# Optimization experiments

Hardware: AMD Instinct MI355X
Metric: run time of the kernel (lower is better)

The kernel has to match this reference:

```python
import jax, jax.numpy as jnp
import numpy as np

D = 2048
H = 16
DK = D // H
B = 2
S = 2048


def setup_inputs() -> dict:
    key = jax.random.key(0)
    ks = jax.random.split(key, 11)
    s = 1.0 / np.sqrt(D)
    inp = {
        "q": jax.random.normal(ks[0], (B, S, D), jnp.float32),
        "k": jax.random.normal(ks[1], (B, S, D), jnp.float32),
        "v": jax.random.normal(ks[2], (B, S, D), jnp.float32),
        "mask": 0,
        "Wq": jax.random.normal(ks[3], (D, D), jnp.float32) * s,
        "bq": jax.random.normal(ks[4], (D,), jnp.float32) * s,
        "Wk": jax.random.normal(ks[5], (D, D), jnp.float32) * s,
        "bk": jax.random.normal(ks[6], (D,), jnp.float32) * s,
        "Wv": jax.random.normal(ks[7], (D, D), jnp.float32) * s,
        "bv": jax.random.normal(ks[8], (D,), jnp.float32) * s,
        "Wo": jax.random.normal(ks[9], (D, D), jnp.float32) * s,
        "bo": jax.random.normal(ks[10], (D,), jnp.float32) * s,
    }
    return inp


def reference(q, k, v, mask, Wq, bq, Wk, bk, Wv, bv, Wo, bo):
    # Linear projections (torch Linear: x @ W.T + b)
    query = q @ Wq.T + bq  # [B,S,D]
    key_ = k @ Wk.T + bk
    value = v @ Wv.T + bv
    # split heads -> [B,S,H,DK]
    query = query.reshape(B, S, H, DK)
    key_ = key_.reshape(B, S, H, DK)
    value = value.reshape(B, S, H, DK)
    # scores [B,H,Sq,Sk]
    scores = jnp.einsum('nqhd,nkhd->nhqk', query, key_)
    if mask:
        # faithful to source: fill where triu(ones, diag=1) == 0 (lower tri incl diag)
        tri = jnp.triu(jnp.ones((S, S), jnp.float32), k=1)
        scores = jnp.where(tri == 0, jnp.float32(-1e20), scores)
    attn = jax.nn.softmax(scores / np.sqrt(DK), axis=3)
    # dropout=0.0 -> identity
    out = jnp.einsum('nhql,nlhd->nqhd', attn, value).reshape(B, S, D)
    return out @ Wo.T + bo
```

## Files before the change

kernel.cpp:

```cpp
#include <hip/hip_runtime.h>
#include <math.h>

typedef unsigned short u16;
typedef u16 u16x8 __attribute__((ext_vector_type(8)));
typedef u16 u16x4 __attribute__((ext_vector_type(4)));
typedef short s16x8 __attribute__((ext_vector_type(8)));
typedef short s16x4 __attribute__((ext_vector_type(4)));
typedef float f32x4 __attribute__((ext_vector_type(4)));

static constexpr int B_ = 2;
static constexpr int S_ = 2048;
static constexpr int D_ = 2048;
static constexpr int H_ = 16;
static constexpr int DK = 128;
static constexpr long long BSD = (long long)B_ * S_ * D_;
static constexpr long long DD  = (long long)D_ * D_;

#if __has_builtin(__builtin_amdgcn_mfma_f32_16x16x32_bf16)
#define HAVE_MFMA32 1
#else
#define HAVE_MFMA32 0
#endif
#if __has_builtin(__builtin_amdgcn_mfma_f32_16x16x16bf16_1k)
#define HAVE_MFMA16 1
#else
#define HAVE_MFMA16 0
#endif

__device__ __forceinline__ u16 f2bf(float f) {
    union { float f; unsigned u; } cv; cv.f = f;
    unsigned u = cv.u;
    return (u16)((u + 0x7fffu + ((u >> 16) & 1u)) >> 16);
}

__device__ __forceinline__ unsigned pack2bf(float a, float b) {
    union { float f; unsigned u; } x, y; x.f = a; y.f = b;
    return ((y.u + 0x8000u) & 0xffff0000u) | ((x.u + 0x8000u) >> 16);
}

__device__ __forceinline__ f32x4 mfma32(f32x4 c, u16x8 a, u16x8 b) {
#if HAVE_MFMA32
    return __builtin_amdgcn_mfma_f32_16x16x32_bf16((s16x8)a, (s16x8)b, c, 0, 0, 0);
#else
    asm volatile("v_mfma_f32_16x16x32_bf16 %0, %1, %2, %0" : "+v"(c) : "v"(a), "v"(b));
    return c;
#endif
}
__device__ __forceinline__ f32x4 mfma16(f32x4 c, u16x4 a, u16x4 b) {
#if HAVE_MFMA16
    return __builtin_amdgcn_mfma_f32_16x16x16bf16_1k((s16x4)a, (s16x4)b, c, 0, 0, 0);
#else
    asm volatile("v_mfma_f32_16x16x16_bf16 %0, %1, %2, %0" : "+v"(c) : "v"(a), "v"(b));
    return c;
#endif
}
__device__ __forceinline__ void fenceB() {
#if !HAVE_MFMA32 || !HAVE_MFMA16
    asm volatile("s_nop 7\ns_nop 7" :::);
#endif
}

__device__ __forceinline__ void glds16(const u16* g, u16* l) {
    __builtin_amdgcn_global_load_lds(
        (const __attribute__((address_space(1))) unsigned int*)g,
        (__attribute__((address_space(3))) unsigned int*)l, 16, 0, 0);
}

__device__ __forceinline__ float fexp2(float x) {
#if __has_builtin(__builtin_amdgcn_exp2f)
    return __builtin_amdgcn_exp2f(x);
#else
    return exp2f(x);
#endif
}

struct CastArgs {
    const float* src[7];
    u16* dst[7];
    int start[8];
};
__global__ __launch_bounds__(256) void cast_all(CastArgs a) {
    int g = blockIdx.x * 256 + threadIdx.x;
    if (g >= a.start[7]) return;
    int seg = 0;
#pragma unroll
    for (int i = 1; i < 7; ++i) seg += (g >= a.start[i]) ? 1 : 0;
    int idx = g - a.start[seg];
    float4 f = ((const float4*)a.src[seg])[idx];
    ushort4 o;
    o.x = f2bf(f.x); o.y = f2bf(f.y); o.z = f2bf(f.z); o.w = f2bf(f.w);
    ((ushort4*)a.dst[seg])[idx] = o;
}

#define GEMM_K64_LOOP(Aptr, Bptr)                                                   \
    for (int k0 = 0; k0 < D_; k0 += 64) {                                           \
        __syncthreads();                                                            \
        _Pragma("unroll")                                                           \
        for (int s = 0; s < 4; ++s) {                                               \
            int slot = s * 256 + t;                                                 \
            int row = slot >> 3;                                                    \
            int c = (t & 7) ^ (row & 7);                                            \
            glds16(Aptr + (m0 + row) * D_ + k0 + c * 8, &As[slot * 8]);             \
        }                                                                           \
        _Pragma("unroll")                                                           \
        for (int s = 0; s < 4; ++s) {                                               \
            int slot = s * 256 + t;                                                 \
            int row = slot >> 3;                                                    \
            int c = (t & 7) ^ (row & 7);                                            \
            glds16(Bptr + (n0 + row) * D_ + k0 + c * 8, &Bs[slot * 8]);             \
        }                                                                           \
        __syncthreads();                                                            \
        u16x8 af[4][2], bf[4][2];                                                   \
        _Pragma("unroll")                                                           \
        for (int i = 0; i < 4; ++i) {                                               \
            int row = wm + i * 16 + l16;                                            \
            _Pragma("unroll")                                                       \
            for (int kk = 0; kk < 2; ++kk)                                          \
                af[i][kk] = *(const u16x8*)(&As[row * 64 +                          \
                                (((kk * 4 + quad) ^ (row & 7)) * 8)]);              \
        }                                                                           \
        _Pragma("unroll")                                                           \
        for (int j = 0; j < 4; ++j) {                                               \
            int row = wn + j * 16 + l16;                                            \
            _Pragma("unroll")                                                       \
            for (int kk = 0; kk < 2; ++kk)                                          \
                bf[j][kk] = *(const u16x8*)(&Bs[row * 64 +                          \
                                (((kk * 4 + quad) ^ (row & 7)) * 8)]);              \
        }                                                                           \
        _Pragma("unroll")                                                           \
        for (int kk = 0; kk < 2; ++kk)                                              \
            _Pragma("unroll")                                                       \
            for (int i = 0; i < 4; ++i)                                             \
                _Pragma("unroll")                                                   \
                for (int j = 0; j < 4; ++j)                                         \
                    acc[i][j] = mfma32(acc[i][j], af[i][kk], bf[j][kk]);            \
    }

struct QkvArgs {
    const u16* X[3];
    const u16* W[3];
    const float* bias[3];
    u16* outQ;
    u16* outK;
    u16* outVt;
    float scaleQ;
};
__global__ __launch_bounds__(256) void qkv_proj(QkvArgs a) {
    __shared__ u16 SM[16384];
    u16* As = SM;
    u16* Bs = SM + 8192;

    const int zsel = blockIdx.z;
    const u16* A = a.X[zsel];
    const u16* Bw = a.W[zsel];
    const float scale = (zsel == 0) ? a.scaleQ : 1.0f;

    const int t = threadIdx.x;
    const int wave = t >> 6, lane = t & 63;
    const int quad = lane >> 4, l16 = lane & 15;
    const int wm = (wave >> 1) * 64;
    const int wn = (wave & 1) * 64;
    const long long m0 = (long long)blockIdx.y * 128;
    const long long n0 = (long long)blockIdx.x * 128;

    f32x4 acc[4][4];
#pragma unroll
    for (int i = 0; i < 4; ++i)
#pragma unroll
        for (int j = 0; j < 4; ++j)
            acc[i][j] = f32x4{0.f, 0.f, 0.f, 0.f};

    GEMM_K64_LOOP(A, Bw)

    fenceB();

    float bs[4];
#pragma unroll
    for (int j = 0; j < 4; ++j)
        bs[j] = a.bias[zsel][(int)n0 + wn + j * 16 + l16];

    if (zsel < 2) {
        u16* C = (zsel == 0) ? a.outQ : a.outK;
#pragma unroll
        for (int p = 0; p < 2; ++p) {
            __syncthreads();
#pragma unroll
            for (int jj = 0; jj < 2; ++jj) {
                int j = p * 2 + jj;
#pragma unroll
                for (int i = 0; i < 4; ++i)
#pragma unroll
                    for (int r = 0; r < 4; ++r) {
                        int row = wm + i * 16 + quad * 4 + r;
                        int lc = (wave & 1) * 32 + jj * 16 + l16;
                        SM[row * 64 + lc] = f2bf((acc[i][j][r] + bs[j]) * scale);
                    }
            }
            __syncthreads();
#pragma unroll
            for (int i = 0; i < 4; ++i) {
                int idx = i * 256 + t;
                int row = idx >> 3, cc = idx & 7;
                u16x8 val = *(const u16x8*)(&SM[row * 64 + cc * 8]);
                long long n = n0 + 32 * p + (cc & 3) * 8 + (cc >> 2) * 64;
                *(u16x8*)(C + (m0 + row) * (long long)D_ + n) = val;
            }
        }
    } else {
        const int h = blockIdx.x;
        const int b = (int)(m0 >> 11);
        const int tok0 = (int)(m0 & 2047);
        const int z = b * 16 + h;
        u16* vt = a.outVt + (long long)z * DK * S_;
#pragma unroll
        for (int p = 0; p < 2; ++p) {
            __syncthreads();
#pragma unroll
            for (int jj = 0; jj < 2; ++jj) {
                int j = p * 2 + jj;
#pragma unroll
                for (int i = 0; i < 4; ++i)
#pragma unroll
                    for (int r = 0; r < 4; ++r) {
                        int row = wm + i * 16 + quad * 4 + r;
                        int lc = (wave & 1) * 32 + jj * 16 + l16;
                        SM[lc * 136 + row] = f2bf(acc[i][j][r] + bs[j]);
                    }
            }
            __syncthreads();
#pragma unroll
            for (int i = 0; i < 4; ++i) {
                int idx = i * 256 + t;
                int lc2 = idx >> 4, cc = idx & 15;
                int d = p * 32 + (lc2 & 31) + (lc2 >> 5) * 64;
                u16x8 val = *(const u16x8*)(&SM[lc2 * 136 + cc * 8]);
                *(u16x8*)(vt + (long long)d * S_ + tok0 + cc * 8) = val;
            }
        }
    }
}

__global__ __launch_bounds__(256) void gemm_out(const u16* __restrict__ Ain,
                                                const u16* __restrict__ Bin,
                                                float* __restrict__ C,
                                                const float* __restrict__ bias) {
    __shared__ u16 SM[16384];
    u16* As = SM;
    u16* Bs = SM + 8192;

    const int t = threadIdx.x;
    const int wave = t >> 6, lane = t & 63;
    const int quad = lane >> 4, l16 = lane & 15;
    const int wm = (wave >> 1) * 64;
    const int wn = (wave & 1) * 64;
    const long long m0 = (long long)blockIdx.y * 128;
    const long long n0 = (long long)blockIdx.x * 128;

    f32x4 acc[4][4];
#pragma unroll
    for (int i = 0; i < 4; ++i)
#pragma unroll
        for (int j = 0; j < 4; ++j)
            acc[i][j] = f32x4{0.f, 0.f, 0.f, 0.f};

    GEMM_K64_LOOP(Ain, Bin)

    fenceB();

    float bs[4];
#pragma unroll
    for (int j = 0; j < 4; ++j)
        bs[j] = bias[(int)n0 + wn + j * 16 + l16];

    float* Cf = (float*)SM;
#pragma unroll
    for (int p = 0; p < 2; ++p) {
        __syncthreads();
#pragma unroll
        for (int jj = 0; jj < 2; ++jj) {
            int j = p * 2 + jj;
#pragma unroll
            for (int i = 0; i < 4; ++i)
#pragma unroll
                for (int r = 0; r < 4; ++r) {
                    int row = wm + i * 16 + quad * 4 + r;
                    int lc = (wave & 1) * 32 + jj * 16 + l16;
                    Cf[row * 64 + lc] = acc[i][j][r] + bs[j];
                }
        }
        __syncthreads();
#pragma unroll
        for (int i = 0; i < 8; ++i) {
            int idx = i * 256 + t;
            int row = idx >> 4, c4 = idx & 15;
            f32x4 val = *(const f32x4*)(&Cf[row * 64 + c4 * 4]);
            long long n = n0 + (c4 >> 3) * 64 + p * 32 + (c4 & 7) * 4;
            *(f32x4*)(C + (m0 + row) * (long long)D_ + n) = val;
        }
    }
}

__global__ __launch_bounds__(256, 2) void flash_attn(const u16* __restrict__ Qb,
                                                     const u16* __restrict__ Kb,
                                                     const u16* __restrict__ Vt,
                                                     u16* __restrict__ Ob) {
    __shared__ u16 Ks[2][64 * 128];
    __shared__ u16 Vs[2][128 * 64];

    const int z  = blockIdx.x;
    const int qt = blockIdx.y;
    const int b  = z >> 4, h = z & 15;
    const int t = threadIdx.x, wave = t >> 6, lane = t & 63;
    const int quad = lane >> 4, l16 = lane & 15;

    const u16* kbase = Kb + (long long)(b * S_) * D_ + h * DK;
    const u16* vbase = Vt + (long long)z * DK * S_;

    u16x8 qf[2][4];
    {
        const u16* qbase = Qb + ((long long)(b * S_ + qt * 128 + wave * 32 + l16)) * D_
                              + h * DK + quad * 8;
#pragma unroll
        for (int jq = 0; jq < 2; ++jq)
#pragma unroll
            for (int kk = 0; kk < 4; ++kk)
                qf[jq][kk] = *(const u16x8*)(qbase + (long long)jq * 16 * D_ + kk * 32);
    }

    f32x4 acc_o[2][8];
#pragma unroll
    for (int jq = 0; jq < 2; ++jq)
#pragma unroll
        for (int jd = 0; jd < 8; ++jd)
            acc_o[jq][jd] = f32x4{0.f, 0.f, 0.f, 0.f};
    float l_[2] = {0.f, 0.f};

    u16x8 vreg[4];

    {
#pragma unroll
        for (int i = 0; i < 4; ++i) {
            int slot = i * 256 + t;
            int row = slot >> 3, c16 = slot & 7;
            vreg[i] = *(const u16x8*)(vbase + (long long)row * S_ + c16 * 8);
        }
#pragma unroll
        for (int i = 0; i < 4; ++i) {
            int slot = i * 256 + t;
            int row = slot >> 4;
            int cs = (slot & 15) ^ (row & 7);
            glds16(kbase + (long long)row * D_ + cs * 8, &Ks[0][slot * 8]);
        }
#pragma unroll
        for (int i = 0; i < 4; ++i) {
            int slot = i * 256 + t;
            int row = slot >> 3, c16 = slot & 7;
            int rm = row & 15;
            u16x4 lo = __builtin_shufflevector(vreg[i], vreg[i], 0, 1, 2, 3);
            u16x4 hi = __builtin_shufflevector(vreg[i], vreg[i], 4, 5, 6, 7);
            *(u16x4*)(&Vs[0][row * 64 + (((2 * c16) ^ rm) * 4)]) = lo;
            *(u16x4*)(&Vs[0][row * 64 + (((2 * c16 + 1) ^ rm) * 4)]) = hi;
        }
    }

    for (int kt = 0; kt < S_ / 64; ++kt) {
        __syncthreads();
        const int p = kt & 1;
        const u16* ks = Ks[p];
        const u16* vs = Vs[p];
        const bool pre = (kt + 1) < (S_ / 64);
        if (pre) {
            const u16* vsrc = vbase + (kt + 1) * 64;
#pragma unroll
            for (int i = 0; i < 4; ++i) {
                int slot = i * 256 + t;
                int row = slot >> 3, c16 = slot & 7;
                vreg[i] = *(const u16x8*)(vsrc + (long long)row * S_ + c16 * 8);
            }
            const u16* ksrc = kbase + (long long)(kt + 1) * 64 * D_;
#pragma unroll
            for (int i = 0; i < 4; ++i) {
                int slot = i * 256 + t;
                int row = slot >> 4;
                int cs = (slot & 15) ^ (row & 7);
                glds16(ksrc + (long long)row * D_ + cs * 8, &Ks[p ^ 1][slot * 8]);
            }
        }

        f32x4 st[4][2];
#pragma unroll
        for (int ik = 0; ik < 4; ++ik)
#pragma unroll
            for (int jq = 0; jq < 2; ++jq)
                st[ik][jq] = f32x4{0.f, 0.f, 0.f, 0.f};
#pragma unroll
        for (int kk = 0; kk < 4; ++kk) {
            u16x8 kf[4];
#pragma unroll
            for (int ik = 0; ik < 4; ++ik) {
                int krow = ik * 16 + l16;
                kf[ik] = *(const u16x8*)(&ks[krow * 128 + (((kk * 4 + quad) ^ (l16 & 7)) * 8)]);
            }
#pragma unroll
            for (int ik = 0; ik < 4; ++ik) {
                st[ik][0] = mfma32(st[ik][0], kf[ik], qf[0][kk]);
                st[ik][1] = mfma32(st[ik][1], kf[ik], qf[1][kk]);
            }
        }
        fenceB();

        if (pre) {
#pragma unroll
            for (int i = 0; i < 4; ++i) {
                int slot = i * 256 + t;
                int row = slot >> 3, c16 = slot & 7;
                int rm = row & 15;
                u16x4 lo = __builtin_shufflevector(vreg[i], vreg[i], 0, 1, 2, 3);
                u16x4 hi = __builtin_shufflevector(vreg[i], vreg[i], 4, 5, 6, 7);
                *(u16x4*)(&Vs[p ^ 1][row * 64 + (((2 * c16) ^ rm) * 4)]) = lo;
                *(u16x4*)(&Vs[p ^ 1][row * 64 + (((2 * c16 + 1) ^ rm) * 4)]) = hi;
            }
        }

        u16x4 pf[4][2];
#pragma unroll
        for (int ik = 0; ik < 4; ++ik)
#pragma unroll
            for (int jq = 0; jq < 2; ++jq) {
                float p0 = fexp2(st[ik][jq][0]);
                float p1 = fexp2(st[ik][jq][1]);
                float p2 = fexp2(st[ik][jq][2]);
                float p3 = fexp2(st[ik][jq][3]);
                l_[jq] += (p0 + p1) + (p2 + p3);
                union { u16x4 v; unsigned u[2]; } pk;
                pk.u[0] = pack2bf(p0, p1);
                pk.u[1] = pack2bf(p2, p3);
                pf[ik][jq] = pk.v;
            }

#pragma unroll
        for (int ik = 0; ik < 4; ++ik) {
            const int kc = ik * 4 + quad;
            u16x4 vf[8];
#pragma unroll
            for (int jd = 0; jd < 8; ++jd) {
                int vrow = jd * 16 + l16;
                vf[jd] = *(const u16x4*)(&vs[vrow * 64 + ((kc ^ l16) * 4)]);
            }
#pragma unroll
            for (int jd = 0; jd < 8; ++jd) {
                acc_o[0][jd] = mfma16(acc_o[0][jd], pf[ik][0], vf[jd]);
                acc_o[1][jd] = mfma16(acc_o[1][jd], pf[ik][1], vf[jd]);
            }
        }
        fenceB();
    }

    float lr[2][4];
#pragma unroll
    for (int jq = 0; jq < 2; ++jq) {
        float s = l_[jq];
        s += __shfl_xor(s, 16, 64);
        s += __shfl_xor(s, 32, 64);
        float inv = 1.f / s;
#pragma unroll
        for (int r = 0; r < 4; ++r)
            lr[jq][r] = __shfl(inv, quad * 20 + r, 64);
    }
    u16* OS = (u16*)Ks;
    __syncthreads();
#pragma unroll
    for (int jq = 0; jq < 2; ++jq)
#pragma unroll
        for (int r = 0; r < 4; ++r) {
            int qloc = wave * 32 + jq * 16 + quad * 4 + r;
#pragma unroll
            for (int jd = 0; jd < 8; ++jd)
                OS[qloc * 128 + jd * 16 + l16] = f2bf(acc_o[jq][jd][r] * lr[jq][r]);
        }
    __syncthreads();
    u16* obase = Ob + ((long long)(b * S_ + qt * 128)) * D_ + h * DK;
#pragma unroll
    for (int i = 0; i < 8; ++i) {
        int idx = i * 256 + t;
        int row = idx >> 4, cc = idx & 15;
        *(u16x8*)(obase + (long long)row * D_ + cc * 8) = *(const u16x8*)(&OS[row * 128 + cc * 8]);
    }
}

extern "C" void kernel_launch(void* const* d_in, const int* in_sizes, int n_in,
                              void* d_out, int out_size, void* d_ws, size_t ws_size,
                              hipStream_t stream) {
    const float* q  = (const float*)d_in[0];
    const float* k  = (const float*)d_in[1];
    const float* v  = (const float*)d_in[2];
    const float* Wq = (const float*)d_in[4];
    const float* bq = (const float*)d_in[5];
    const float* Wk = (const float*)d_in[6];
    const float* bk = (const float*)d_in[7];
    const float* Wv = (const float*)d_in[8];
    const float* bv = (const float*)d_in[9];
    const float* Wo = (const float*)d_in[10];
    const float* bo = (const float*)d_in[11];
    float* out = (float*)d_out;

    u16* ws = (u16*)d_ws;
    u16* xq  = ws; ws += BSD;
    u16* xk  = ws; ws += BSD;
    u16* xv  = ws; ws += BSD;
    u16* wqb = ws; ws += DD;
    u16* wkb = ws; ws += DD;
    u16* wvb = ws; ws += DD;
    u16* wob = ws; ws += DD;
    u16* Qb  = ws; ws += BSD;
    u16* Kb  = ws; ws += BSD;
    u16* Vt  = ws; ws += BSD;
    u16* Ob  = ws; ws += BSD;

    const float q_scale = (float)(0.08838834764831845 * 1.4426950408889634);

    {
        CastArgs a;
        const float* srcs[7] = {q, k, v, Wq, Wk, Wv, Wo};
        u16* dsts[7] = {xq, xk, xv, wqb, wkb, wvb, wob};
        int n4s[7] = {(int)(BSD / 4), (int)(BSD / 4), (int)(BSD / 4),
                      (int)(DD / 4), (int)(DD / 4), (int)(DD / 4), (int)(DD / 4)};
        int acc = 0;
        for (int i = 0; i < 7; ++i) { a.src[i] = srcs[i]; a.dst[i] = dsts[i]; a.start[i] = acc; acc += n4s[i]; }
        a.start[7] = acc;
        cast_all<<<(acc + 255) / 256, 256, 0, stream>>>(a);
    }

    {
        QkvArgs a;
        a.X[0] = xq;  a.X[1] = xk;  a.X[2] = xv;
        a.W[0] = wqb; a.W[1] = wkb; a.W[2] = wvb;
        a.bias[0] = bq; a.bias[1] = bk; a.bias[2] = bv;
        a.outQ = Qb; a.outK = Kb; a.outVt = Vt;
        a.scaleQ = q_scale;
        qkv_proj<<<dim3(D_ / 128, (B_ * S_) / 128, 3), 256, 0, stream>>>(a);
    }

    flash_attn<<<dim3(B_ * H_, S_ / 128), 256, 0, stream>>>(Qb, Kb, Vt, Ob);

    gemm_out<<<dim3(D_ / 128, (B_ * S_) / 128), 256, 0, stream>>>(Ob, wob, out, bo);
}
```

Baseline: 446.7 us.

## Rewrite QKV projection as 256x256-tile, 8-wave double-buffered GEMM with swizzled LDS

Replaces the 128x128 QKV projection kernel with a 512-thread kernel computing 256x256 output tiles. It double-buffers A and B tiles in 128 KB of LDS via direct global-to-LDS loads with an XOR swizzle, and interleaves the loads with MFMA phases using explicit waitcnt, barriers and setprio. The aim is more operand reuse per loaded byte, fewer bank conflicts and overlap of memory with math. The trade-off is high register and LDS pressure: there are 32 accumulators per wave, and 128 KB of LDS per block probably means one block per CU. The epilogues are also rewritten for the larger tile.

```diff
diff --git a/kernel.cpp b/kernel.cpp
--- a/kernel.cpp
+++ b/kernel.cpp
@@ -74,6 +74,16 @@
 #endif
 }
 
+__device__ __forceinline__ void cfence() { asm volatile("" ::: "memory"); }
+__device__ __forceinline__ void barrier8() {
+    cfence();
+    __builtin_amdgcn_s_barrier();
+    cfence();
+}
+#define LGKM0() do { asm volatile("s_waitcnt lgkmcnt(0)" ::: "memory"); \
+                     __builtin_amdgcn_sched_barrier(0); } while (0)
+#define VMC(N)  asm volatile("s_waitcnt vmcnt(" #N ")" ::: "memory")
+
 struct CastArgs {
     const float* src[7];
     u16* dst[7];
@@ -145,96 +155,188 @@
     u16* outVt;
     float scaleQ;
 };
-__global__ __launch_bounds__(256) void qkv_proj(QkvArgs a) {
-    __shared__ u16 SM[16384];
-    u16* As = SM;
-    u16* Bs = SM + 8192;
+
+#define STAGE_HALF(LDS, GBASE)                                                      \
+    _Pragma("unroll")                                                               \
+    for (int jj = 0; jj < 2; ++jj) {                                                \
+        int slot = jj * 512 + t;                                                    \
+        int row = slot >> 3, c = slot & 7;                                          \
+        glds16((GBASE) + (long long)row * D_ + ((c ^ (row & 7)) * 8),               \
+               (LDS) + slot * 8);                                                   \
+    }
+
+#define RD_A(QM, LDSA)                                                              \
+    _Pragma("unroll")                                                               \
+    for (int i2 = 0; i2 < 4; ++i2) {                                                \
+        int row = wm128 + (QM) * 64 + i2 * 16 + l16;                                \
+        _Pragma("unroll")                                                           \
+        for (int kk = 0; kk < 2; ++kk)                                              \
+            af[(QM) * 4 + i2][kk] = *(const u16x8*)(&(LDSA)[row * 64 +              \
+                                (((kk * 4 + quad) ^ (row & 7)) * 8)]);              \
+    }
+
+#define RD_B(QN, LDSB)                                                              \
+    _Pragma("unroll")                                                               \
+    for (int j2 = 0; j2 < 2; ++j2) {                                                \
+        int row = wn64 + (QN) * 32 + j2 * 16 + l16;                                 \
+        _Pragma("unroll")                                                           \
+        for (int kk = 0; kk < 2; ++kk)                                              \
+            bf[j2][kk] = *(const u16x8*)(&(LDSB)[row * 64 +                         \
+                                (((kk * 4 + quad) ^ (row & 7)) * 8)]);              \
+    }
+
+#define MM(QM, QN)                                                                  \
+    __builtin_amdgcn_s_setprio(1);                                                  \
+    _Pragma("unroll")                                                               \
+    for (int kk = 0; kk < 2; ++kk)                                                  \
+        _Pragma("unroll")                                                           \
+        for (int i2 = 0; i2 < 4; ++i2)                                              \
+            _Pragma("unroll")                                                       \
+            for (int j2 = 0; j2 < 2; ++j2)                                          \
+                acc[(QM) * 4 + i2][(QN) * 2 + j2] =                                 \
+                    mfma32(acc[(QM) * 4 + i2][(QN) * 2 + j2],                       \
+                           af[(QM) * 4 + i2][kk], bf[j2][kk]);                      \
+    __builtin_amdgcn_s_setprio(0);
+
+__global__ __launch_bounds__(512, 2) void qkv_proj8(QkvArgs a) {
+    __shared__ u16 SM8[65536];
+    u16* const As0 = SM8;
+    u16* const As1 = SM8 + 16384;
+    u16* const Bs0 = SM8 + 32768;
+    u16* const Bs1 = SM8 + 49152;
 
     const int zsel = blockIdx.z;
-    const u16* A = a.X[zsel];
-    const u16* Bw = a.W[zsel];
-    const float scale = (zsel == 0) ? a.scaleQ : 1.0f;
+    const u16* __restrict__ Ag = a.X[zsel];
+    const u16* __restrict__ Bg = a.W[zsel];
 
     const int t = threadIdx.x;
-    const int wave = t >> 6, lane = t & 63;
+    const int lane = t & 63;
     const int quad = lane >> 4, l16 = lane & 15;
-    const int wm = (wave >> 1) * 64;
-    const int wn = (wave & 1) * 64;
-    const long long m0 = (long long)blockIdx.y * 128;
-    const long long n0 = (long long)blockIdx.x * 128;
-
-    f32x4 acc[4][4];
-#pragma unroll
-    for (int i = 0; i < 4; ++i)
+    const int wave = t >> 6;
+    const int wm128 = (wave >> 2) * 128;
+    const int wn64  = (wave & 3) * 64;
+    const long long m0 = (long long)blockIdx.y * 256;
+    const long long n0 = (long long)blockIdx.x * 256;
+
+    f32x4 acc[8][4];
+#pragma unroll
+    for (int i = 0; i < 8; ++i)
 #pragma unroll
         for (int j = 0; j < 4; ++j)
             acc[i][j] = f32x4{0.f, 0.f, 0.f, 0.f};
 
-    GEMM_K64_LOOP(A, Bw)
-
+    u16x8 af[8][2];
+    u16x8 bf[2][2];
+
+    STAGE_HALF(As0,         Ag + m0 * D_)
+    STAGE_HALF(As0 + 8192,  Ag + (m0 + 128) * D_)
+    STAGE_HALF(Bs0,         Bg + n0 * D_)
+    STAGE_HALF(Bs0 + 8192,  Bg + (n0 + 128) * D_)
+    STAGE_HALF(As1,         Ag + m0 * D_ + 64)
+    STAGE_HALF(As1 + 8192,  Ag + (m0 + 128) * D_ + 64)
+    VMC(4);
+    barrier8();
+
+#pragma unroll 1
+    for (int it = 0; it < 16; ++it) {
+        const int E = 2 * it;
+        const bool more = (it < 15);
+        const long long kO  = (long long)(E + 1) * 64;
+        const long long kE2 = (long long)(E + 2) * 64;
+        const long long kO2 = (long long)(E + 3) * 64;
+
+        RD_A(0, As0) RD_B(0, Bs0)
+        STAGE_HALF(Bs1,        Bg + n0 * D_ + kO)
+        barrier8(); LGKM0(); MM(0, 0) barrier8();
+
+        RD_A(1, As0) RD_B(1, Bs0)
+        STAGE_HALF(Bs1 + 8192, Bg + (n0 + 128) * D_ + kO)
+        barrier8(); LGKM0(); MM(0, 1) barrier8();
+
+        RD_B(0, Bs0)
+        if (more) { STAGE_HALF(As0,        Ag + m0 * D_ + kE2) }
+        barrier8(); LGKM0(); MM(1, 0) barrier8();
+
+        RD_B(1, Bs0)
+        if (more) { STAGE_HALF(As0 + 8192, Ag + (m0 + 128) * D_ + kE2) }
+        barrier8(); LGKM0(); MM(1, 1)
+        if (more) { VMC(4); } else { VMC(0); }
+        barrier8();
+
+        RD_A(0, As1) RD_B(0, Bs1)
+        if (more) { STAGE_HALF(Bs0,        Bg + n0 * D_ + kE2) }
+        barrier8(); LGKM0(); MM(0, 0) barrier8();
+
+        RD_A(1, As1) RD_B(1, Bs1)
+        if (more) { STAGE_HALF(Bs0 + 8192, Bg + (n0 + 128) * D_ + kE2) }
+        barrier8(); LGKM0(); MM(0, 1) barrier8();
+
+        RD_B(0, Bs1)
+        if (more) { STAGE_HALF(As1,        Ag + m0 * D_ + kO2) }
+        barrier8(); LGKM0(); MM(1, 0) barrier8();
+
+        RD_B(1, Bs1)
+        if (more) { STAGE_HALF(As1 + 8192, Ag + (m0 + 128) * D_ + kO2) }
+        barrier8(); LGKM0(); MM(1, 1)
+        if (more) { VMC(4); }
+        barrier8();
+    }
     fenceB();
 
     float bs[4];
 #pragma unroll
     for (int j = 0; j < 4; ++j)
-        bs[j] = a.bias[zsel][(int)n0 + wn + j * 16 + l16];
+        bs[j] = a.bias[zsel][(int)n0 + wn64 + j * 16 + l16];
 
     if (zsel < 2) {
+        const float scale = (zsel == 0) ? a.scaleQ : 1.0f;
         u16* C = (zsel == 0) ? a.outQ : a.outK;
 #pragma unroll
-        for (int p = 0; p < 2; ++p) {
-            __syncthreads();
-#pragma unroll
-            for (int jj = 0; jj < 2; ++jj) {
-                int j = p * 2 + jj;
-#pragma unroll
-                for (int i = 0; i < 4; ++i)
-#pragma unroll
-                    for (int r = 0; r < 4; ++r) {
-                        int row = wm + i * 16 + quad * 4 + r;
-                        int lc = (wave & 1) * 32 + jj * 16 + l16;
-                        SM[row * 64 + lc] = f2bf((acc[i][j][r] + bs[j]) * scale);
-                    }
-            }
-            __syncthreads();
-#pragma unroll
-            for (int i = 0; i < 4; ++i) {
-                int idx = i * 256 + t;
-                int row = idx >> 3, cc = idx & 7;
-                u16x8 val = *(const u16x8*)(&SM[row * 64 + cc * 8]);
-                long long n = n0 + 32 * p + (cc & 3) * 8 + (cc >> 2) * 64;
-                *(u16x8*)(C + (m0 + row) * (long long)D_ + n) = val;
-            }
+        for (int i = 0; i < 8; ++i)
+#pragma unroll
+            for (int j = 0; j < 4; ++j)
+#pragma unroll
+                for (int r = 0; r < 4; ++r) {
+                    int row = wm128 + i * 16 + quad * 4 + r;
+                    int col = wn64 + j * 16 + l16;
+                    SM8[row * 256 + col] = f2bf((acc[i][j][r] + bs[j]) * scale);
+                }
+        barrier8();
+#pragma unroll
+        for (int s = 0; s < 16; ++s) {
+            int idx = s * 512 + t;
+            int row = idx >> 5, c = idx & 31;
+            *(u16x8*)(C + (m0 + row) * (long long)D_ + n0 + c * 8) =
+                *(const u16x8*)(&SM8[row * 256 + c * 8]);
         }
     } else {
-        const int h = blockIdx.x;
-        const int b = (int)(m0 >> 11);
+        const int h0 = (int)(n0 >> 7);
+        const int bb = (int)(m0 >> 11);
         const int tok0 = (int)(m0 & 2047);
-        const int z = b * 16 + h;
-        u16* vt = a.outVt + (long long)z * DK * S_;
-#pragma unroll
-        for (int p = 0; p < 2; ++p) {
-            __syncthreads();
-#pragma unroll
-            for (int jj = 0; jj < 2; ++jj) {
-                int j = p * 2 + jj;
-#pragma unroll
-                for (int i = 0; i < 4; ++i)
-#pragma unroll
-                    for (int r = 0; r < 4; ++r) {
-                        int row = wm + i * 16 + quad * 4 + r;
-                        int lc = (wave & 1) * 32 + jj * 16 + l16;
-                        SM[lc * 136 + row] = f2bf(acc[i][j][r] + bs[j]);
-                    }
-            }
-            __syncthreads();
-#pragma unroll
-            for (int i = 0; i < 4; ++i) {
-                int idx = i * 256 + t;
-                int lc2 = idx >> 4, cc = idx & 15;
-                int d = p * 32 + (lc2 & 31) + (lc2 >> 5) * 64;
-                u16x8 val = *(const u16x8*)(&SM[lc2 * 136 + cc * 8]);
-                *(u16x8*)(vt + (long long)d * S_ + tok0 + cc * 8) = val;
+#pragma unroll
+        for (int pass = 0; pass < 2; ++pass) {
+            barrier8();
+            if ((wn64 >> 7) == pass) {
+                int cb = wn64 & 127;
+#pragma unroll
+                for (int i = 0; i < 8; ++i)
+#pragma unroll
+                    for (int j = 0; j < 4; ++j)
+#pragma unroll
+                        for (int r = 0; r < 4; ++r) {
+                            int row = wm128 + i * 16 + quad * 4 + r;
+                            int d = cb + j * 16 + l16;
+                            SM8[d * 264 + row] = f2bf(acc[i][j][r] + bs[j]);
+                        }
+            }
+            barrier8();
+            u16* vt = a.outVt + (long long)(bb * 16 + h0 + pass) * DK * S_;
+#pragma unroll
+            for (int s = 0; s < 8; ++s) {
+                int idx = s * 512 + t;
+                int d = idx >> 5, tc = idx & 31;
+                *(u16x8*)(vt + (long long)d * S_ + tok0 + tc * 8) =
+                    *(const u16x8*)(&SM8[d * 264 + tc * 8]);
             }
         }
     }
@@ -538,7 +640,7 @@
         a.bias[0] = bq; a.bias[1] = bk; a.bias[2] = bv;
         a.outQ = Qb; a.outK = Kb; a.outVt = Vt;
         a.scaleQ = q_scale;
-        qkv_proj<<<dim3(D_ / 128, (B_ * S_) / 128, 3), 256, 0, stream>>>(a);
+        qkv_proj8<<<dim3(D_ / 256, (B_ * S_) / 256, 3), 512, 0, stream>>>(a);
     }
 
     flash_attn<<<dim3(B_ * H_, S_ / 128), 256, 0, stream>>>(Qb, Kb, Vt, Ob);
```

New measurement: 448.8 us. About the same (+0.5%).
